# Kernel tuning notes

Measured on AMD Instinct MI355X. Metric: run time of the kernel, lower is better.

The kernel has to match this reference:

```python
import jax, jax.numpy as jnp
import numpy as np

H = 1024
B = 32
S = 2048
N_LAYERS = 2


def setup_inputs() -> dict:
    key = jax.random.key(0)
    k1, k2, k3, k4, k5 = jax.random.split(key, 5)
    hidden = jax.random.normal(k1, (N_LAYERS, B, H), dtype=jnp.float32)
    encoder_outputs = jax.random.normal(k2, (B, S, H), dtype=jnp.float32)
    # nn.Linear(2H, H): weight [H, 2H], bias [H]
    W_attn = jax.random.normal(k3, (H, 2 * H), dtype=jnp.float32) * (1.0 / np.sqrt(2 * H))
    b_attn = jax.random.normal(k4, (H,), dtype=jnp.float32) * 0.01
    v = jax.random.uniform(k5, (H,), dtype=jnp.float32)
    return {"hidden": hidden, "encoder_outputs": encoder_outputs,
            "W_attn": W_attn, "b_attn": b_attn, "v": v}


def reference(hidden, encoder_outputs, W_attn, b_attn, v):
    # hidden: [L, B, H] -> take last layer [B, H]
    h = hidden[-1]
    # Split the linear over the concat dim: cat([h_exp, enc]) @ W.T ==
    #   h @ W[:, :H].T  (broadcast over S)  +  enc @ W[:, H:].T
    Wh = W_attn[:, :H]   # [H, H] acts on decoder hidden
    We = W_attn[:, H:]   # [H, H] acts on encoder outputs
    proj_h = jnp.einsum('bh,oh->bo', h, Wh) + b_attn          # [B, H]
    proj_e = jnp.einsum('bsh,oh->bso', encoder_outputs, We)   # [B, S, H]
    energy = jnp.tanh(proj_e + proj_h[:, None, :])            # [B, S, H]
    scores = jnp.einsum('bsh,h->bs', energy, v)               # [B, S]
    attn_weights = jax.nn.softmax(scores, axis=1)             # [B, S]
    context = jnp.einsum('bs,bsh->bh', attn_weights, encoder_outputs)  # [B, H]
    return (context, attn_weights)
```

## Files before the change

kernel.cpp:

```cpp
#include <hip/hip_runtime.h>
#include <hip/hip_bf16.h>

#define H 1024
#define B 32
#define S 2048

typedef __attribute__((ext_vector_type(8))) _Float16 h8;
typedef __attribute__((ext_vector_type(4))) _Float16 h4;
typedef __attribute__((ext_vector_type(4))) float f32x4;

__device__ __forceinline__ float fast_tanh(float x) {
    float a = __builtin_fabsf(x);
    float e = __expf(2.0f * a);
    float r = 1.0f - 2.0f / (e + 1.0f);
    return __builtin_copysignf(r, x);
}

__device__ __forceinline__ void gload_lds16(const void* g, void* l) {
    __builtin_amdgcn_global_load_lds(
        (const __attribute__((address_space(1))) unsigned int*)g,
        (__attribute__((address_space(3))) unsigned int*)l, 16, 0, 0);
}

__global__ __launch_bounds__(256) void proj_h_kernel(
    const float* __restrict__ hidden, const float* __restrict__ W,
    const float* __restrict__ b_attn, float* __restrict__ ph)
{
    const int b = blockIdx.y;
    const int tid = threadIdx.x;
    __shared__ float hs[H];
    const float4* hr = (const float4*)(hidden + (size_t)(B + b) * H);
    ((float4*)hs)[tid] = hr[tid];
    __syncthreads();
    const int w = tid >> 6, lane = tid & 63;
    const int o = blockIdx.x * 4 + w;
    const float* wr = W + (size_t)o * (2 * H);
    float acc = 0.f;
    #pragma unroll
    for (int i = 0; i < 16; ++i) {
        const int k = i * 64 + lane;
        acc += wr[k] * hs[k];
    }
    #pragma unroll
    for (int off = 32; off; off >>= 1) acc += __shfl_xor(acc, off);
    if (lane == 0) ph[b * H + o] = acc + b_attn[o];
}

__global__ __launch_bounds__(256) void conv_We(
    const float* __restrict__ W, _Float16* __restrict__ We_h)
{
    const int o = blockIdx.x;
    const int t = threadIdx.x;
    float4 f = *(const float4*)(W + (size_t)o * 2048 + 1024 + t * 4);
    h4 hv = {(_Float16)f.x, (_Float16)f.y, (_Float16)f.z, (_Float16)f.w};
    *(h4*)(We_h + (size_t)o * 1024 + t * 4) = hv;
}

__global__ __launch_bounds__(256, 3) void score_v5(
    const float* __restrict__ enc, const _Float16* __restrict__ We_h,
    const float* __restrict__ ph, const float* __restrict__ v,
    float* __restrict__ partial)
{
    __shared__ float    As[128 * 64];
    __shared__ _Float16 Bs[128 * 64];
    __shared__ float slds[256];

    const int tid = threadIdx.x;
    const int bid = blockIdx.x;
    const int x  = bid & 7;
    const int ii = bid >> 3;
    const int nb = ii & 7;
    const int mt = (ii >> 3) * 8 + x;
    const int b  = mt >> 4;

    const int lane = tid & 63;
    const int wid  = tid >> 6;
    const int wm = wid >> 1, wn = wid & 1;
    const int l15 = lane & 15, lg = lane >> 4;

    const int a_rsub = lane >> 4;
    const int a_sl   = lane & 15;
    const int b_rsub = lane >> 3;
    const int b_sl   = lane & 7;

    f32x4 acc[4][4];
    #pragma unroll
    for (int mi = 0; mi < 4; ++mi)
        #pragma unroll
        for (int ni = 0; ni < 4; ++ni) acc[mi][ni] = (f32x4){0.f, 0.f, 0.f, 0.f};

    for (int kt = 0; kt < 16; ++kt) {
        const int k0 = kt * 64;
        __syncthreads();
        #pragma unroll
        for (int i = 0; i < 8; ++i) {
            const int c = i * 4 + wid;
            const int r = c * 4 + a_rsub;
            gload_lds16(enc + (size_t)(mt * 128 + r) * H + k0 + ((a_sl ^ (r & 15)) * 4),
                        (char*)As + c * 1024);
        }
        #pragma unroll
        for (int q = 0; q < 4; ++q) {
            const int n  = q * 32 + wid * 8 + b_rsub;
            const int gn = nb * 128 + n;
            gload_lds16(We_h + (size_t)gn * H + k0 + ((b_sl ^ (n & 7)) * 8),
                        (char*)Bs + (q * 32 + wid * 8) * 128);
        }
        __syncthreads();
        #pragma unroll
        for (int ks = 0; ks < 2; ++ks) {
            h8 ah[4], bh[4];
            #pragma unroll
            for (int mi = 0; mi < 4; ++mi) {
                const int r  = wm * 64 + mi * 16 + l15;
                const int s0 = ks * 8 + lg * 2;
                f32x4 f0 = *(const f32x4*)((const char*)As + r * 256 + ((s0 ^ (r & 15)) * 16));
                f32x4 f1 = *(const f32x4*)((const char*)As + r * 256 + (((s0 + 1) ^ (r & 15)) * 16));
                ah[mi] = (h8){(_Float16)f0[0], (_Float16)f0[1], (_Float16)f0[2], (_Float16)f0[3],
                              (_Float16)f1[0], (_Float16)f1[1], (_Float16)f1[2], (_Float16)f1[3]};
            }
            #pragma unroll
            for (int ni = 0; ni < 4; ++ni) {
                const int r  = wn * 64 + ni * 16 + l15;
                const int sl = ks * 4 + lg;
                bh[ni] = *(const h8*)((const char*)Bs + r * 128 + ((sl ^ (r & 7)) * 16));
            }
            #pragma unroll
            for (int mi = 0; mi < 4; ++mi)
                #pragma unroll
                for (int ni = 0; ni < 4; ++ni)
                    acc[mi][ni] = __builtin_amdgcn_mfma_f32_16x16x32_f16(
                        ah[mi], bh[ni], acc[mi][ni], 0, 0, 0);
        }
    }

    float vreg[4], preg[4];
    #pragma unroll
    for (int ni = 0; ni < 4; ++ni) {
        const int gcol = nb * 128 + wn * 64 + ni * 16 + l15;
        vreg[ni] = v[gcol];
        preg[ni] = ph[b * H + gcol];
    }
    #pragma unroll
    for (int mi = 0; mi < 4; ++mi) {
        #pragma unroll
        for (int j = 0; j < 4; ++j) {
            float p = 0.f;
            #pragma unroll
            for (int ni = 0; ni < 4; ++ni)
                p += vreg[ni] * fast_tanh(acc[mi][ni][j] + preg[ni]);
            p += __shfl_xor(p, 1); p += __shfl_xor(p, 2);
            p += __shfl_xor(p, 4); p += __shfl_xor(p, 8);
            if (l15 == 0)
                slds[wn * 128 + wm * 64 + mi * 16 + lg * 4 + j] = p;
        }
    }
    __syncthreads();
    if (tid < 128)
        partial[(size_t)nb * (B * S) + mt * 128 + tid] = slds[tid] + slds[128 + tid];
}

__global__ __launch_bounds__(256) void score_v4f(
    const float* __restrict__ enc, const float* __restrict__ Wf,
    const float* __restrict__ ph, const float* __restrict__ v,
    float* __restrict__ partial)
{
    __shared__ _Float16 As[128 * 64];
    __shared__ _Float16 Bs[128 * 64];
    __shared__ float slds[256];
    const int tid = threadIdx.x;
    const int bid = blockIdx.x;
    const int x  = bid & 7;
    const int ii = bid >> 3;
    const int nb = ii & 7;
    const int mt = (ii >> 3) * 8 + x;
    const int b  = mt >> 4;
    const int lane = tid & 63;
    const int wid  = tid >> 6;
    const int wm = wid >> 1, wn = wid & 1;
    const int l15 = lane & 15, lg = lane >> 4;
    const int arow  = tid >> 3;
    const int aslot = tid & 7;
    f32x4 acc[4][4];
    #pragma unroll
    for (int mi = 0; mi < 4; ++mi)
        #pragma unroll
        for (int ni = 0; ni < 4; ++ni) acc[mi][ni] = (f32x4){0.f, 0.f, 0.f, 0.f};
    for (int kt = 0; kt < 16; ++kt) {
        const int k0 = kt * 64;
        __syncthreads();
        #pragma unroll
        for (int p = 0; p < 4; ++p) {
            const int m = p * 32 + arow;
            const float* src = enc + (size_t)(mt * 128 + m) * H + k0 + aslot * 8;
            float4 f0 = *(const float4*)src;
            float4 f1 = *(const float4*)(src + 4);
            h8 hv = {(_Float16)f0.x, (_Float16)f0.y, (_Float16)f0.z, (_Float16)f0.w,
                     (_Float16)f1.x, (_Float16)f1.y, (_Float16)f1.z, (_Float16)f1.w};
            *(h8*)((char*)As + m * 128 + ((aslot ^ (m & 7)) * 16)) = hv;
        }
        #pragma unroll
        for (int p = 0; p < 4; ++p) {
            const int n  = p * 32 + arow;
            const int gn = nb * 128 + n;
            const float* src = Wf + (size_t)gn * 2048 + 1024 + k0 + aslot * 8;
            float4 f0 = *(const float4*)src;
            float4 f1 = *(const float4*)(src + 4);
            h8 hv = {(_Float16)f0.x, (_Float16)f0.y, (_Float16)f0.z, (_Float16)f0.w,
                     (_Float16)f1.x, (_Float16)f1.y, (_Float16)f1.z, (_Float16)f1.w};
            *(h8*)((char*)Bs + n * 128 + ((aslot ^ (n & 7)) * 16)) = hv;
        }
        __syncthreads();
        #pragma unroll
        for (int ks = 0; ks < 2; ++ks) {
            h8 ah[4], bh[4];
            const int sl = ks * 4 + lg;
            #pragma unroll
            for (int mi = 0; mi < 4; ++mi) {
                const int r = wm * 64 + mi * 16 + l15;
                ah[mi] = *(const h8*)((char*)As + r * 128 + 16 * (sl ^ (r & 7)));
            }
            #pragma unroll
            for (int ni = 0; ni < 4; ++ni) {
                const int r = wn * 64 + ni * 16 + l15;
                bh[ni] = *(const h8*)((char*)Bs + r * 128 + 16 * (sl ^ (r & 7)));
            }
            #pragma unroll
            for (int mi = 0; mi < 4; ++mi)
                #pragma unroll
                for (int ni = 0; ni < 4; ++ni)
                    acc[mi][ni] = __builtin_amdgcn_mfma_f32_16x16x32_f16(
                        ah[mi], bh[ni], acc[mi][ni], 0, 0, 0);
        }
    }
    float vreg[4], preg[4];
    #pragma unroll
    for (int ni = 0; ni < 4; ++ni) {
        const int gcol = nb * 128 + wn * 64 + ni * 16 + l15;
        vreg[ni] = v[gcol];
        preg[ni] = ph[b * H + gcol];
    }
    #pragma unroll
    for (int mi = 0; mi < 4; ++mi) {
        #pragma unroll
        for (int j = 0; j < 4; ++j) {
            float p = 0.f;
            #pragma unroll
            for (int ni = 0; ni < 4; ++ni)
                p += vreg[ni] * fast_tanh(acc[mi][ni][j] + preg[ni]);
            p += __shfl_xor(p, 1); p += __shfl_xor(p, 2);
            p += __shfl_xor(p, 4); p += __shfl_xor(p, 8);
            if (l15 == 0)
                slds[wn * 128 + wm * 64 + mi * 16 + lg * 4 + j] = p;
        }
    }
    __syncthreads();
    if (tid < 128)
        partial[(size_t)nb * (B * S) + mt * 128 + tid] = slds[tid] + slds[128 + tid];
}

__global__ __launch_bounds__(256) void softmax_kernel(
    const float* __restrict__ partial, float* __restrict__ attn)
{
    const int b = blockIdx.x, tid = threadIdx.x;
    float xv[8];
    float m = -1e30f;
    #pragma unroll
    for (int i = 0; i < 8; ++i) {
        float s = 0.f;
        #pragma unroll
        for (int nb = 0; nb < 8; ++nb)
            s += partial[(size_t)nb * (B * S) + b * S + tid + i * 256];
        xv[i] = s;
        m = fmaxf(m, s);
    }
    #pragma unroll
    for (int off = 32; off; off >>= 1) m = fmaxf(m, __shfl_xor(m, off));
    __shared__ float wred[4], wsum[4];
    const int w = tid >> 6;
    if ((tid & 63) == 0) wred[w] = m;
    __syncthreads();
    const float M = fmaxf(fmaxf(wred[0], wred[1]), fmaxf(wred[2], wred[3]));
    float s = 0.f;
    #pragma unroll
    for (int i = 0; i < 8; ++i) { xv[i] = expf(xv[i] - M); s += xv[i]; }
    #pragma unroll
    for (int off = 32; off; off >>= 1) s += __shfl_xor(s, off);
    if ((tid & 63) == 0) wsum[w] = s;
    __syncthreads();
    const float inv = 1.f / (wsum[0] + wsum[1] + wsum[2] + wsum[3]);
    #pragma unroll
    for (int i = 0; i < 8; ++i) attn[b * S + tid + i * 256] = xv[i] * inv;
}

__global__ __launch_bounds__(256) void ctx_partial(
    const float* __restrict__ enc, const float* __restrict__ attn,
    float* __restrict__ part, int rows)
{
    const int sc = blockIdx.x;
    const int b  = blockIdx.y;
    const int tid = threadIdx.x;
    const float* encb = enc + ((size_t)b * S + (size_t)sc * rows) * H;
    const float* wb = attn + b * S + sc * rows;
    __shared__ float wl[256];
    if (tid < rows) wl[tid] = wb[tid];
    __syncthreads();
    float4 acc = {0.f, 0.f, 0.f, 0.f};
    for (int s = 0; s < rows; ++s) {
        const float wgt = wl[s];
        const float4 e = *(const float4*)(encb + (size_t)s * H + tid * 4);
        acc.x += wgt * e.x; acc.y += wgt * e.y; acc.z += wgt * e.z; acc.w += wgt * e.w;
    }
    ((float4*)(part + ((size_t)(sc * B + b)) * H))[tid] = acc;
}

__global__ __launch_bounds__(256) void ctx_reduce(
    const float* __restrict__ part, float* __restrict__ ctx, int nch)
{
    const int i = blockIdx.x * 256 + threadIdx.x;
    float s = 0.f;
    for (int c = 0; c < nch; ++c) s += part[(size_t)c * (B * H) + i];
    ctx[i] = s;
}

extern "C" void kernel_launch(void* const* d_in, const int* in_sizes, int n_in,
                              void* d_out, int out_size, void* d_ws, size_t ws_size,
                              hipStream_t stream) {
    const float* hidden = (const float*)d_in[0];
    const float* enc    = (const float*)d_in[1];
    const float* W      = (const float*)d_in[2];
    const float* b_attn = (const float*)d_in[3];
    const float* v      = (const float*)d_in[4];
    float* ctx  = (float*)d_out;
    float* attn = ctx + B * H;
    float* ws      = (float*)d_ws;
    float* region  = ws;
    float* ph      = ws + 524288;
    _Float16* We_h = (_Float16*)(ws + 524288 + 32768);

    proj_h_kernel<<<dim3(H / 4, B), 256, 0, stream>>>(hidden, W, b_attn, ph);

    const size_t need_primary = (size_t)(524288 + 32768 + 524288) * 4;
    if (ws_size >= need_primary) {
        conv_We<<<1024, 256, 0, stream>>>(W, We_h);
        score_v5<<<4096, 256, 0, stream>>>(enc, We_h, ph, v, region);
    } else {
        score_v4f<<<4096, 256, 0, stream>>>(enc, W, ph, v, region);
    }
    softmax_kernel<<<dim3(B), 256, 0, stream>>>(region, attn);
    ctx_partial<<<dim3(16, B), 256, 0, stream>>>(enc, attn, region, 128);
    ctx_reduce<<<dim3((B * H) / 256), 256, 0, stream>>>(region, ctx, 16);
}
```

Before: 266.1 us.

## Replace score GEMM with 256x256-tile double-buffered kernel converting A to fp16 in LDS

```diff
diff --git a/kernel.cpp b/kernel.cpp
--- a/kernel.cpp
+++ b/kernel.cpp
@@ -22,6 +22,11 @@
         (__attribute__((address_space(3))) unsigned int*)l, 16, 0, 0);
 }
 
+__device__ __forceinline__ h8 cvt8(float4 a, float4 b) {
+    return (h8){(_Float16)a.x, (_Float16)a.y, (_Float16)a.z, (_Float16)a.w,
+                (_Float16)b.x, (_Float16)b.y, (_Float16)b.z, (_Float16)b.w};
+}
+
 __global__ __launch_bounds__(256) void proj_h_kernel(
     const float* __restrict__ hidden, const float* __restrict__ W,
     const float* __restrict__ b_attn, float* __restrict__ ph)
@@ -56,93 +61,113 @@
     *(h4*)(We_h + (size_t)o * 1024 + t * 4) = hv;
 }
 
-__global__ __launch_bounds__(256, 3) void score_v5(
+#define V7_LDS 69632
+__global__ __launch_bounds__(512, 2) void score_v7(
     const float* __restrict__ enc, const _Float16* __restrict__ We_h,
     const float* __restrict__ ph, const float* __restrict__ v,
     float* __restrict__ partial)
 {
-    __shared__ float    As[128 * 64];
-    __shared__ _Float16 Bs[128 * 64];
-    __shared__ float slds[256];
+    extern __shared__ __align__(16) char smem[];
+    float* slds = (float*)(smem + 65536);
 
     const int tid = threadIdx.x;
     const int bid = blockIdx.x;
-    const int x  = bid & 7;
-    const int ii = bid >> 3;
-    const int nb = ii & 7;
-    const int mt = (ii >> 3) * 8 + x;
-    const int b  = mt >> 4;
-
-    const int lane = tid & 63;
-    const int wid  = tid >> 6;
-    const int wm = wid >> 1, wn = wid & 1;
+    const int xcd = bid & 7, idx = bid >> 3;
+    const int lin = xcd * 128 + idx;
+    const int nt = lin & 3, mt = lin >> 2;
+    const int bb = mt >> 3;
+
+    const int lane = tid & 63, wid = tid >> 6;
+    const int wm = wid >> 2, wn = wid & 3;
     const int l15 = lane & 15, lg = lane >> 4;
 
-    const int a_rsub = lane >> 4;
-    const int a_sl   = lane & 15;
-    const int b_rsub = lane >> 3;
-    const int b_sl   = lane & 7;
-
-    f32x4 acc[4][4];
-    #pragma unroll
-    for (int mi = 0; mi < 4; ++mi)
+    const int ar = tid >> 1, ah = tid & 1;
+    const int agA = (ar ^ (ar >> 2)) & 3;
+    const int br = tid >> 2, bs = tid & 3;
+    const float*    Ag = enc + ((size_t)(mt * 256) + ar) * H + ah * 16;
+    const _Float16* Bg = We_h + (size_t)(nt * 256) * H;
+
+    f32x4 acc[8][4];
+    #pragma unroll
+    for (int mi = 0; mi < 8; ++mi)
         #pragma unroll
         for (int ni = 0; ni < 4; ++ni) acc[mi][ni] = (f32x4){0.f, 0.f, 0.f, 0.f};
 
-    for (int kt = 0; kt < 16; ++kt) {
-        const int k0 = kt * 64;
-        __syncthreads();
-        #pragma unroll
-        for (int i = 0; i < 8; ++i) {
-            const int c = i * 4 + wid;
-            const int r = c * 4 + a_rsub;
-            gload_lds16(enc + (size_t)(mt * 128 + r) * H + k0 + ((a_sl ^ (r & 15)) * 4),
-                        (char*)As + c * 1024);
-        }
-        #pragma unroll
-        for (int q = 0; q < 4; ++q) {
-            const int n  = q * 32 + wid * 8 + b_rsub;
-            const int gn = nb * 128 + n;
-            gload_lds16(We_h + (size_t)gn * H + k0 + ((b_sl ^ (n & 7)) * 8),
-                        (char*)Bs + (q * 32 + wid * 8) * 128);
-        }
-        __syncthreads();
-        #pragma unroll
-        for (int ks = 0; ks < 2; ++ks) {
-            h8 ah[4], bh[4];
-            #pragma unroll
-            for (int mi = 0; mi < 4; ++mi) {
-                const int r  = wm * 64 + mi * 16 + l15;
-                const int s0 = ks * 8 + lg * 2;
-                f32x4 f0 = *(const f32x4*)((const char*)As + r * 256 + ((s0 ^ (r & 15)) * 16));
-                f32x4 f1 = *(const f32x4*)((const char*)As + r * 256 + (((s0 + 1) ^ (r & 15)) * 16));
-                ah[mi] = (h8){(_Float16)f0[0], (_Float16)f0[1], (_Float16)f0[2], (_Float16)f0[3],
-                              (_Float16)f1[0], (_Float16)f1[1], (_Float16)f1[2], (_Float16)f1[3]};
+    #define STAGE_B(buf, k0, j) { \
+        const int n = (j) * 128 + br; \
+        gload_lds16(Bg + (size_t)n * H + (k0) + ((bs ^ ((n ^ (n >> 2)) & 3)) * 8), \
+                    smem + 32768 + (buf) * 16384 + n * 64 + bs * 16); }
+    #define WRITE_A(buf, f) { \
+        h8 w0 = cvt8(f[0], f[1]); h8 w1 = cvt8(f[2], f[3]); \
+        char* dst = smem + (buf) * 16384 + ar * 64; \
+        *(h8*)(dst + (((ah * 2)     ^ agA) * 16)) = w0; \
+        *(h8*)(dst + (((ah * 2 + 1) ^ agA) * 16)) = w1; }
+
+    {
+        float4 f[4];
+        #pragma unroll
+        for (int i = 0; i < 4; ++i) f[i] = *(const float4*)(Ag + i * 4);
+        WRITE_A(0, f)
+        STAGE_B(0, 0, 0)
+        STAGE_B(0, 0, 1)
+    }
+    __syncthreads();
+
+    #pragma unroll 2
+    for (int t = 0; t < 32; ++t) {
+        const int cur = t & 1, nxt = cur ^ 1;
+        const char* Ac = smem + cur * 16384;
+        const char* Bc = smem + 32768 + cur * 16384;
+        const int k0n = (t + 1) * 32;
+
+        float4 apre[4];
+        if (t < 31) {
+            const float* asrc = Ag + (size_t)k0n;
+            #pragma unroll
+            for (int i = 0; i < 4; ++i) apre[i] = *(const float4*)(asrc + i * 4);
+            STAGE_B(nxt, k0n, 0)
+            STAGE_B(nxt, k0n, 1)
+        }
+        __builtin_amdgcn_sched_barrier(0);
+
+        h8 bfr[4];
+        #pragma unroll
+        for (int ni = 0; ni < 4; ++ni) {
+            const int n = wn * 64 + ni * 16 + l15;
+            bfr[ni] = *(const h8*)(Bc + n * 64 + ((lg ^ ((n ^ (n >> 2)) & 3)) * 16));
+        }
+        #pragma unroll
+        for (int mh = 0; mh < 2; ++mh) {
+            h8 af[4];
+            #pragma unroll
+            for (int fi = 0; fi < 4; ++fi) {
+                const int r = wm * 128 + (mh * 4 + fi) * 16 + l15;
+                af[fi] = *(const h8*)(Ac + r * 64 + ((lg ^ ((r ^ (r >> 2)) & 3)) * 16));
             }
-            #pragma unroll
-            for (int ni = 0; ni < 4; ++ni) {
-                const int r  = wn * 64 + ni * 16 + l15;
-                const int sl = ks * 4 + lg;
-                bh[ni] = *(const h8*)((const char*)Bs + r * 128 + ((sl ^ (r & 7)) * 16));
-            }
-            #pragma unroll
-            for (int mi = 0; mi < 4; ++mi)
+            __builtin_amdgcn_s_setprio(1);
+            #pragma unroll
+            for (int fi = 0; fi < 4; ++fi)
                 #pragma unroll
                 for (int ni = 0; ni < 4; ++ni)
-                    acc[mi][ni] = __builtin_amdgcn_mfma_f32_16x16x32_f16(
-                        ah[mi], bh[ni], acc[mi][ni], 0, 0, 0);
-        }
-    }
+                    acc[mh * 4 + fi][ni] = __builtin_amdgcn_mfma_f32_16x16x32_f16(
+                        af[fi], bfr[ni], acc[mh * 4 + fi][ni], 0, 0, 0);
+            __builtin_amdgcn_s_setprio(0);
+        }
+        if (t < 31) WRITE_A(nxt, apre)
+        __syncthreads();
+    }
+    #undef STAGE_B
+    #undef WRITE_A
 
     float vreg[4], preg[4];
     #pragma unroll
     for (int ni = 0; ni < 4; ++ni) {
-        const int gcol = nb * 128 + wn * 64 + ni * 16 + l15;
+        const int gcol = nt * 256 + wn * 64 + ni * 16 + l15;
         vreg[ni] = v[gcol];
-        preg[ni] = ph[b * H + gcol];
-    }
-    #pragma unroll
-    for (int mi = 0; mi < 4; ++mi) {
+        preg[ni] = ph[bb * H + gcol];
+    }
+    #pragma unroll
+    for (int mi = 0; mi < 8; ++mi) {
         #pragma unroll
         for (int j = 0; j < 4; ++j) {
             float p = 0.f;
@@ -152,12 +177,13 @@
             p += __shfl_xor(p, 1); p += __shfl_xor(p, 2);
             p += __shfl_xor(p, 4); p += __shfl_xor(p, 8);
             if (l15 == 0)
-                slds[wn * 128 + wm * 64 + mi * 16 + lg * 4 + j] = p;
-        }
-    }
-    __syncthreads();
-    if (tid < 128)
-        partial[(size_t)nb * (B * S) + mt * 128 + tid] = slds[tid] + slds[128 + tid];
+                slds[wn * 256 + wm * 128 + mi * 16 + lg * 4 + j] = p;
+        }
+    }
+    __syncthreads();
+    if (tid < 256)
+        partial[(size_t)nt * (B * S) + mt * 256 + tid] =
+            slds[tid] + slds[256 + tid] + slds[512 + tid] + slds[768 + tid];
 }
 
 __global__ __launch_bounds__(256) void score_v4f(
@@ -195,9 +221,7 @@
             const float* src = enc + (size_t)(mt * 128 + m) * H + k0 + aslot * 8;
             float4 f0 = *(const float4*)src;
             float4 f1 = *(const float4*)(src + 4);
-            h8 hv = {(_Float16)f0.x, (_Float16)f0.y, (_Float16)f0.z, (_Float16)f0.w,
-                     (_Float16)f1.x, (_Float16)f1.y, (_Float16)f1.z, (_Float16)f1.w};
-            *(h8*)((char*)As + m * 128 + ((aslot ^ (m & 7)) * 16)) = hv;
+            *(h8*)((char*)As + m * 128 + ((aslot ^ (m & 7)) * 16)) = cvt8(f0, f1);
         }
         #pragma unroll
         for (int p = 0; p < 4; ++p) {
@@ -206,9 +230,7 @@
             const float* src = Wf + (size_t)gn * 2048 + 1024 + k0 + aslot * 8;
             float4 f0 = *(const float4*)src;
             float4 f1 = *(const float4*)(src + 4);
-            h8 hv = {(_Float16)f0.x, (_Float16)f0.y, (_Float16)f0.z, (_Float16)f0.w,
-                     (_Float16)f1.x, (_Float16)f1.y, (_Float16)f1.z, (_Float16)f1.w};
-            *(h8*)((char*)Bs + n * 128 + ((aslot ^ (n & 7)) * 16)) = hv;
+            *(h8*)((char*)Bs + n * 128 + ((aslot ^ (n & 7)) * 16)) = cvt8(f0, f1);
         }
         __syncthreads();
         #pragma unroll
@@ -260,7 +282,7 @@
 }
 
 __global__ __launch_bounds__(256) void softmax_kernel(
-    const float* __restrict__ partial, float* __restrict__ attn)
+    const float* __restrict__ partial, float* __restrict__ attn, int nparts)
 {
     const int b = blockIdx.x, tid = threadIdx.x;
     float xv[8];
@@ -268,8 +290,7 @@
     #pragma unroll
     for (int i = 0; i < 8; ++i) {
         float s = 0.f;
-        #pragma unroll
-        for (int nb = 0; nb < 8; ++nb)
+        for (int nb = 0; nb < nparts; ++nb)
             s += partial[(size_t)nb * (B * S) + b * S + tid + i * 256];
         xv[i] = s;
         m = fmaxf(m, s);
@@ -343,11 +364,14 @@
     const size_t need_primary = (size_t)(524288 + 32768 + 524288) * 4;
     if (ws_size >= need_primary) {
         conv_We<<<1024, 256, 0, stream>>>(W, We_h);
-        score_v5<<<4096, 256, 0, stream>>>(enc, We_h, ph, v, region);
+        hipFuncSetAttribute((const void*)score_v7,
+                            hipFuncAttributeMaxDynamicSharedMemorySize, V7_LDS);
+        score_v7<<<1024, 512, V7_LDS, stream>>>(enc, We_h, ph, v, region);
+        softmax_kernel<<<dim3(B), 256, 0, stream>>>(region, attn, 4);
     } else {
         score_v4f<<<4096, 256, 0, stream>>>(enc, W, ph, v, region);
-    }
-    softmax_kernel<<<dim3(B), 256, 0, stream>>>(region, attn);
+        softmax_kernel<<<dim3(B), 256, 0, stream>>>(region, attn, 8);
+    }
     ctx_partial<<<dim3(16, B), 256, 0, stream>>>(enc, attn, region, 128);
     ctx_reduce<<<dim3((B * H) / 256), 256, 0, stream>>>(region, ctx, 16);
 }
```

New measurement: 312.1 us. 1.17x slower.

## Double-buffer score GEMM with register-staged fp16 A tiles and K=32 steps

Applied to the files above, without the earlier changes.

```diff
diff --git a/kernel.cpp b/kernel.cpp
--- a/kernel.cpp
+++ b/kernel.cpp
@@ -22,6 +22,11 @@
         (__attribute__((address_space(3))) unsigned int*)l, 16, 0, 0);
 }
 
+__device__ __forceinline__ h8 cvt8(float4 a, float4 b) {
+    return (h8){(_Float16)a.x, (_Float16)a.y, (_Float16)a.z, (_Float16)a.w,
+                (_Float16)b.x, (_Float16)b.y, (_Float16)b.z, (_Float16)b.w};
+}
+
 __global__ __launch_bounds__(256) void proj_h_kernel(
     const float* __restrict__ hidden, const float* __restrict__ W,
     const float* __restrict__ b_attn, float* __restrict__ ph)
@@ -56,13 +61,13 @@
     *(h4*)(We_h + (size_t)o * 1024 + t * 4) = hv;
 }
 
-__global__ __launch_bounds__(256, 3) void score_v5(
+__global__ __launch_bounds__(256, 4) void score_v8(
     const float* __restrict__ enc, const _Float16* __restrict__ We_h,
     const float* __restrict__ ph, const float* __restrict__ v,
     float* __restrict__ partial)
 {
-    __shared__ float    As[128 * 64];
-    __shared__ _Float16 Bs[128 * 64];
+    __shared__ _Float16 Als[2][128][32];
+    __shared__ _Float16 Bls[2][128][32];
     __shared__ float slds[256];
 
     const int tid = threadIdx.x;
@@ -78,10 +83,11 @@
     const int wm = wid >> 1, wn = wid & 1;
     const int l15 = lane & 15, lg = lane >> 4;
 
-    const int a_rsub = lane >> 4;
-    const int a_sl   = lane & 15;
-    const int b_rsub = lane >> 3;
-    const int b_sl   = lane & 7;
+    const int ar = tid >> 1, ahalf = tid & 1;
+    const int aswz = (ar >> 1) & 3;
+    const float* Ag = enc + (size_t)(mt * 128 + ar) * H + ahalf * 16;
+    const int bn0 = tid >> 2, bs = tid & 3;
+    const _Float16* Bg = We_h + (size_t)(nb * 128) * H;
 
     f32x4 acc[4][4];
     #pragma unroll
@@ -89,50 +95,100 @@
         #pragma unroll
         for (int ni = 0; ni < 4; ++ni) acc[mi][ni] = (f32x4){0.f, 0.f, 0.f, 0.f};
 
-    for (int kt = 0; kt < 16; ++kt) {
-        const int k0 = kt * 64;
-        __syncthreads();
-        #pragma unroll
-        for (int i = 0; i < 8; ++i) {
-            const int c = i * 4 + wid;
-            const int r = c * 4 + a_rsub;
-            gload_lds16(enc + (size_t)(mt * 128 + r) * H + k0 + ((a_sl ^ (r & 15)) * 4),
-                        (char*)As + c * 1024);
-        }
-        #pragma unroll
-        for (int q = 0; q < 4; ++q) {
-            const int n  = q * 32 + wid * 8 + b_rsub;
-            const int gn = nb * 128 + n;
-            gload_lds16(We_h + (size_t)gn * H + k0 + ((b_sl ^ (n & 7)) * 8),
-                        (char*)Bs + (q * 32 + wid * 8) * 128);
-        }
-        __syncthreads();
-        #pragma unroll
-        for (int ks = 0; ks < 2; ++ks) {
-            h8 ah[4], bh[4];
-            #pragma unroll
-            for (int mi = 0; mi < 4; ++mi) {
-                const int r  = wm * 64 + mi * 16 + l15;
-                const int s0 = ks * 8 + lg * 2;
-                f32x4 f0 = *(const f32x4*)((const char*)As + r * 256 + ((s0 ^ (r & 15)) * 16));
-                f32x4 f1 = *(const f32x4*)((const char*)As + r * 256 + (((s0 + 1) ^ (r & 15)) * 16));
-                ah[mi] = (h8){(_Float16)f0[0], (_Float16)f0[1], (_Float16)f0[2], (_Float16)f0[3],
-                              (_Float16)f1[0], (_Float16)f1[1], (_Float16)f1[2], (_Float16)f1[3]};
-            }
-            #pragma unroll
-            for (int ni = 0; ni < 4; ++ni) {
-                const int r  = wn * 64 + ni * 16 + l15;
-                const int sl = ks * 4 + lg;
-                bh[ni] = *(const h8*)((const char*)Bs + r * 128 + ((sl ^ (r & 7)) * 16));
-            }
-            #pragma unroll
-            for (int mi = 0; mi < 4; ++mi)
-                #pragma unroll
-                for (int ni = 0; ni < 4; ++ni)
-                    acc[mi][ni] = __builtin_amdgcn_mfma_f32_16x16x32_f16(
-                        ah[mi], bh[ni], acc[mi][ni], 0, 0, 0);
-        }
-    }
+    #define STAGE_B(buf, k0) { \
+        _Pragma("unroll") \
+        for (int j = 0; j < 2; ++j) { \
+            const int n = j * 64 + bn0; \
+            gload_lds16(Bg + (size_t)n * H + (k0) + ((bs ^ ((n >> 1) & 3)) * 8), \
+                        (char*)&Bls[buf][j * 64 + wid * 16][0] - (size_t)((wid * 16 - (tid >> 2) + (tid >> 2)) - wid * 16) * 0 + (size_t)0); \
+        } }
+    #undef STAGE_B
+    #define STAGE_B(buf, k0) { \
+        _Pragma("unroll") \
+        for (int j = 0; j < 2; ++j) { \
+            const int n = j * 64 + bn0; \
+            gload_lds16(Bg + (size_t)n * H + (k0) + ((bs ^ ((n >> 1) & 3)) * 8), \
+                        (char*)&Bls[buf][0][0] + (j * 64 + wid * 16) * 64 + (lane * 16)); \
+        } }
+
+    #define WRITE_A(buf, f0, f1, f2, f3) { \
+        h8 w0 = cvt8(f0, f1), w1 = cvt8(f2, f3); \
+        char* dst = (char*)&Als[buf][0][0] + ar * 64; \
+        *(h8*)(dst + (((ahalf * 2)     ^ aswz) * 16)) = w0; \
+        *(h8*)(dst + (((ahalf * 2 + 1) ^ aswz) * 16)) = w1; }
+
+    {
+        float4 a0 = *(const float4*)(Ag + 0);
+        float4 a1 = *(const float4*)(Ag + 4);
+        float4 a2 = *(const float4*)(Ag + 8);
+        float4 a3 = *(const float4*)(Ag + 12);
+        STAGE_B(0, 0)
+        asm volatile("s_waitcnt vmcnt(2)" ::: "memory");
+        WRITE_A(0, a0, a1, a2, a3)
+        asm volatile("s_waitcnt lgkmcnt(0)" ::: "memory");
+        __builtin_amdgcn_s_barrier();
+    }
+
+    for (int t = 0; t < 31; ++t) {
+        const int cur = t & 1, nxt = cur ^ 1;
+        const int k0n = (t + 1) * 32;
+        float4 a0 = *(const float4*)(Ag + k0n);
+        float4 a1 = *(const float4*)(Ag + k0n + 4);
+        float4 a2 = *(const float4*)(Ag + k0n + 8);
+        float4 a3 = *(const float4*)(Ag + k0n + 12);
+        STAGE_B(nxt, k0n)
+        asm volatile("s_waitcnt vmcnt(6)" ::: "memory");
+        __builtin_amdgcn_s_barrier();
+        __builtin_amdgcn_sched_barrier(0);
+
+        h8 af[4], bf[4];
+        #pragma unroll
+        for (int mi = 0; mi < 4; ++mi) {
+            const int r = wm * 64 + mi * 16 + l15;
+            af[mi] = *(const h8*)((const char*)&Als[cur][0][0] + r * 64 + ((lg ^ ((r >> 1) & 3)) * 16));
+        }
+        #pragma unroll
+        for (int ni = 0; ni < 4; ++ni) {
+            const int n = wn * 64 + ni * 16 + l15;
+            bf[ni] = *(const h8*)((const char*)&Bls[cur][0][0] + n * 64 + ((lg ^ ((n >> 1) & 3)) * 16));
+        }
+        __builtin_amdgcn_s_setprio(1);
+        #pragma unroll
+        for (int mi = 0; mi < 4; ++mi)
+            #pragma unroll
+            for (int ni = 0; ni < 4; ++ni)
+                acc[mi][ni] = __builtin_amdgcn_mfma_f32_16x16x32_f16(
+                    af[mi], bf[ni], acc[mi][ni], 0, 0, 0);
+        __builtin_amdgcn_s_setprio(0);
+
+        asm volatile("s_waitcnt vmcnt(2)" ::: "memory");
+        WRITE_A(nxt, a0, a1, a2, a3)
+        asm volatile("s_waitcnt lgkmcnt(0)" ::: "memory");
+        __builtin_amdgcn_s_barrier();
+    }
+    {
+        asm volatile("s_waitcnt vmcnt(0)" ::: "memory");
+        __builtin_amdgcn_s_barrier();
+        h8 af[4], bf[4];
+        #pragma unroll
+        for (int mi = 0; mi < 4; ++mi) {
+            const int r = wm * 64 + mi * 16 + l15;
+            af[mi] = *(const h8*)((const char*)&Als[1][0][0] + r * 64 + ((lg ^ ((r >> 1) & 3)) * 16));
+        }
+        #pragma unroll
+        for (int ni = 0; ni < 4; ++ni) {
+            const int n = wn * 64 + ni * 16 + l15;
+            bf[ni] = *(const h8*)((const char*)&Bls[1][0][0] + n * 64 + ((lg ^ ((n >> 1) & 3)) * 16));
+        }
+        #pragma unroll
+        for (int mi = 0; mi < 4; ++mi)
+            #pragma unroll
+            for (int ni = 0; ni < 4; ++ni)
+                acc[mi][ni] = __builtin_amdgcn_mfma_f32_16x16x32_f16(
+                    af[mi], bf[ni], acc[mi][ni], 0, 0, 0);
+    }
+    #undef STAGE_B
+    #undef WRITE_A
 
     float vreg[4], preg[4];
     #pragma unroll
@@ -195,9 +251,7 @@
             const float* src = enc + (size_t)(mt * 128 + m) * H + k0 + aslot * 8;
             float4 f0 = *(const float4*)src;
             float4 f1 = *(const float4*)(src + 4);
-            h8 hv = {(_Float16)f0.x, (_Float16)f0.y, (_Float16)f0.z, (_Float16)f0.w,
-                     (_Float16)f1.x, (_Float16)f1.y, (_Float16)f1.z, (_Float16)f1.w};
-            *(h8*)((char*)As + m * 128 + ((aslot ^ (m & 7)) * 16)) = hv;
+            *(h8*)((char*)As + m * 128 + ((aslot ^ (m & 7)) * 16)) = cvt8(f0, f1);
         }
         #pragma unroll
         for (int p = 0; p < 4; ++p) {
@@ -206,9 +260,7 @@
             const float* src = Wf + (size_t)gn * 2048 + 1024 + k0 + aslot * 8;
             float4 f0 = *(const float4*)src;
             float4 f1 = *(const float4*)(src + 4);
-            h8 hv = {(_Float16)f0.x, (_Float16)f0.y, (_Float16)f0.z, (_Float16)f0.w,
-                     (_Float16)f1.x, (_Float16)f1.y, (_Float16)f1.z, (_Float16)f1.w};
-            *(h8*)((char*)Bs + n * 128 + ((aslot ^ (n & 7)) * 16)) = hv;
+            *(h8*)((char*)Bs + n * 128 + ((aslot ^ (n & 7)) * 16)) = cvt8(f0, f1);
         }
         __syncthreads();
         #pragma unroll
@@ -343,7 +395,7 @@
     const size_t need_primary = (size_t)(524288 + 32768 + 524288) * 4;
     if (ws_size >= need_primary) {
         conv_We<<<1024, 256, 0, stream>>>(W, We_h);
-        score_v5<<<4096, 256, 0, stream>>>(enc, We_h, ph, v, region);
+        score_v8<<<4096, 256, 0, stream>>>(enc, We_h, ph, v, region);
     } else {
         score_v4f<<<4096, 256, 0, stream>>>(enc, W, ph, v, region);
     }
```

Measured after the change: 377.5 us. +41.8%, slower.

## Double-buffer score GEMM LDS tiles with K=32 stages and async prefetch

Applied to the files above, without the earlier changes.

```diff
diff --git a/kernel.cpp b/kernel.cpp
--- a/kernel.cpp
+++ b/kernel.cpp
@@ -22,6 +22,15 @@
         (__attribute__((address_space(3))) unsigned int*)l, 16, 0, 0);
 }
 
+__device__ __forceinline__ h8 cvt8(f32x4 a, f32x4 b) {
+    return (h8){(_Float16)a[0], (_Float16)a[1], (_Float16)a[2], (_Float16)a[3],
+                (_Float16)b[0], (_Float16)b[1], (_Float16)b[2], (_Float16)b[3]};
+}
+__device__ __forceinline__ h8 cvt8f(float4 a, float4 b) {
+    return (h8){(_Float16)a.x, (_Float16)a.y, (_Float16)a.z, (_Float16)a.w,
+                (_Float16)b.x, (_Float16)b.y, (_Float16)b.z, (_Float16)b.w};
+}
+
 __global__ __launch_bounds__(256) void proj_h_kernel(
     const float* __restrict__ hidden, const float* __restrict__ W,
     const float* __restrict__ b_attn, float* __restrict__ ph)
@@ -56,13 +65,13 @@
     *(h4*)(We_h + (size_t)o * 1024 + t * 4) = hv;
 }
 
-__global__ __launch_bounds__(256, 3) void score_v5(
+__global__ __launch_bounds__(256, 3) void score_v10(
     const float* __restrict__ enc, const _Float16* __restrict__ We_h,
     const float* __restrict__ ph, const float* __restrict__ v,
     float* __restrict__ partial)
 {
-    __shared__ float    As[128 * 64];
-    __shared__ _Float16 Bs[128 * 64];
+    __shared__ float    Als[2][128][32];
+    __shared__ _Float16 Bls[2][128][32];
     __shared__ float slds[256];
 
     const int tid = threadIdx.x;
@@ -78,10 +87,26 @@
     const int wm = wid >> 1, wn = wid & 1;
     const int l15 = lane & 15, lg = lane >> 4;
 
-    const int a_rsub = lane >> 4;
-    const int a_sl   = lane & 15;
-    const int b_rsub = lane >> 3;
-    const int b_sl   = lane & 7;
+    const int a_n0 = wid * 8 + (lane >> 3);
+    const int a_s  = lane & 7;
+    const int b_n0 = wid * 16 + (lane >> 2);
+    const int b_s  = lane & 3;
+    const float*    Ag = enc  + (size_t)(mt * 128) * H;
+    const _Float16* Bg = We_h + (size_t)(nb * 128) * H;
+
+    #define STAGE(buf, k0) { \
+        _Pragma("unroll") \
+        for (int q = 0; q < 4; ++q) { \
+            const int n = q * 32 + a_n0; \
+            gload_lds16(Ag + (size_t)n * H + (k0) + ((a_s ^ (n & 7)) * 4), \
+                        (char*)&Als[buf][0][0] + (q * 32 + wid * 8) * 128); \
+        } \
+        _Pragma("unroll") \
+        for (int q = 0; q < 2; ++q) { \
+            const int n = q * 64 + b_n0; \
+            gload_lds16(Bg + (size_t)n * H + (k0) + ((b_s ^ ((n >> 1) & 3)) * 8), \
+                        (char*)&Bls[buf][0][0] + (q * 64 + wid * 16) * 64); \
+        } }
 
     f32x4 acc[4][4];
     #pragma unroll
@@ -89,50 +114,38 @@
         #pragma unroll
         for (int ni = 0; ni < 4; ++ni) acc[mi][ni] = (f32x4){0.f, 0.f, 0.f, 0.f};
 
-    for (int kt = 0; kt < 16; ++kt) {
-        const int k0 = kt * 64;
+    STAGE(0, 0)
+    __syncthreads();
+
+    for (int t = 0; t < 32; ++t) {
+        const int cur = t & 1;
+        if (t < 31) STAGE(cur ^ 1, (t + 1) * 32)
+
+        h8 af[4], bf[4];
+        #pragma unroll
+        for (int mi = 0; mi < 4; ++mi) {
+            const int r = wm * 64 + mi * 16 + l15;
+            const char* rowp = (const char*)&Als[cur][r][0];
+            f32x4 f0 = *(const f32x4*)(rowp + (((lg * 2)     ^ (r & 7)) * 16));
+            f32x4 f1 = *(const f32x4*)(rowp + (((lg * 2 + 1) ^ (r & 7)) * 16));
+            af[mi] = cvt8(f0, f1);
+        }
+        #pragma unroll
+        for (int ni = 0; ni < 4; ++ni) {
+            const int n = wn * 64 + ni * 16 + l15;
+            bf[ni] = *(const h8*)((const char*)&Bls[cur][n][0] +
+                                  ((lg ^ ((n >> 1) & 3)) * 16));
+        }
+        #pragma unroll
+        for (int mi = 0; mi < 4; ++mi)
+            #pragma unroll
+            for (int ni = 0; ni < 4; ++ni)
+                acc[mi][ni] = __builtin_amdgcn_mfma_f32_16x16x32_f16(
+                    af[mi], bf[ni], acc[mi][ni], 0, 0, 0);
+
         __syncthreads();
-        #pragma unroll
-        for (int i = 0; i < 8; ++i) {
-            const int c = i * 4 + wid;
-            const int r = c * 4 + a_rsub;
-            gload_lds16(enc + (size_t)(mt * 128 + r) * H + k0 + ((a_sl ^ (r & 15)) * 4),
-                        (char*)As + c * 1024);
-        }
-        #pragma unroll
-        for (int q = 0; q < 4; ++q) {
-            const int n  = q * 32 + wid * 8 + b_rsub;
-            const int gn = nb * 128 + n;
-            gload_lds16(We_h + (size_t)gn * H + k0 + ((b_sl ^ (n & 7)) * 8),
-                        (char*)Bs + (q * 32 + wid * 8) * 128);
-        }
-        __syncthreads();
-        #pragma unroll
-        for (int ks = 0; ks < 2; ++ks) {
-            h8 ah[4], bh[4];
-            #pragma unroll
-            for (int mi = 0; mi < 4; ++mi) {
-                const int r  = wm * 64 + mi * 16 + l15;
-                const int s0 = ks * 8 + lg * 2;
-                f32x4 f0 = *(const f32x4*)((const char*)As + r * 256 + ((s0 ^ (r & 15)) * 16));
-                f32x4 f1 = *(const f32x4*)((const char*)As + r * 256 + (((s0 + 1) ^ (r & 15)) * 16));
-                ah[mi] = (h8){(_Float16)f0[0], (_Float16)f0[1], (_Float16)f0[2], (_Float16)f0[3],
-                              (_Float16)f1[0], (_Float16)f1[1], (_Float16)f1[2], (_Float16)f1[3]};
-            }
-            #pragma unroll
-            for (int ni = 0; ni < 4; ++ni) {
-                const int r  = wn * 64 + ni * 16 + l15;
-                const int sl = ks * 4 + lg;
-                bh[ni] = *(const h8*)((const char*)Bs + r * 128 + ((sl ^ (r & 7)) * 16));
-            }
-            #pragma unroll
-            for (int mi = 0; mi < 4; ++mi)
-                #pragma unroll
-                for (int ni = 0; ni < 4; ++ni)
-                    acc[mi][ni] = __builtin_amdgcn_mfma_f32_16x16x32_f16(
-                        ah[mi], bh[ni], acc[mi][ni], 0, 0, 0);
-        }
-    }
+    }
+    #undef STAGE
 
     float vreg[4], preg[4];
     #pragma unroll
@@ -195,9 +208,7 @@
             const float* src = enc + (size_t)(mt * 128 + m) * H + k0 + aslot * 8;
             float4 f0 = *(const float4*)src;
             float4 f1 = *(const float4*)(src + 4);
-            h8 hv = {(_Float16)f0.x, (_Float16)f0.y, (_Float16)f0.z, (_Float16)f0.w,
-                     (_Float16)f1.x, (_Float16)f1.y, (_Float16)f1.z, (_Float16)f1.w};
-            *(h8*)((char*)As + m * 128 + ((aslot ^ (m & 7)) * 16)) = hv;
+            *(h8*)((char*)As + m * 128 + ((aslot ^ (m & 7)) * 16)) = cvt8f(f0, f1);
         }
         #pragma unroll
         for (int p = 0; p < 4; ++p) {
@@ -206,9 +217,7 @@
             const float* src = Wf + (size_t)gn * 2048 + 1024 + k0 + aslot * 8;
             float4 f0 = *(const float4*)src;
             float4 f1 = *(const float4*)(src + 4);
-            h8 hv = {(_Float16)f0.x, (_Float16)f0.y, (_Float16)f0.z, (_Float16)f0.w,
-                     (_Float16)f1.x, (_Float16)f1.y, (_Float16)f1.z, (_Float16)f1.w};
-            *(h8*)((char*)Bs + n * 128 + ((aslot ^ (n & 7)) * 16)) = hv;
+            *(h8*)((char*)Bs + n * 128 + ((aslot ^ (n & 7)) * 16)) = cvt8f(f0, f1);
         }
         __syncthreads();
         #pragma unroll
@@ -343,7 +352,7 @@
     const size_t need_primary = (size_t)(524288 + 32768 + 524288) * 4;
     if (ws_size >= need_primary) {
         conv_We<<<1024, 256, 0, stream>>>(W, We_h);
-        score_v5<<<4096, 256, 0, stream>>>(enc, We_h, ph, v, region);
+        score_v10<<<4096, 256, 0, stream>>>(enc, We_h, ph, v, region);
     } else {
         score_v4f<<<4096, 256, 0, stream>>>(enc, W, ph, v, region);
     }
```

After: 331.1 us. 24.4% more time.
